# Optimization experiments

Measured on AMD Instinct MI355X. Metric: run time of the kernel, lower is better.

## Reference

```python
import jax, jax.numpy as jnp
import numpy as np

UNITS = 1024
HEADS = 16
DEPTH = UNITS // HEADS          # 64
REL_LEN = 64 + 1                # max_relative_position + 1
M = 2 * REL_LEN - 1             # 129 relative buckets (bidirectional)
B, L = 4, 1024


def setup_inputs() -> dict:
    key = jax.random.key(0)
    ks = jax.random.split(key, 8)
    s = 0.02
    x = jax.random.normal(ks[0], (B, L, UNITS), jnp.float32)
    wq = jax.random.normal(ks[1], (UNITS, UNITS), jnp.float32) * s
    wk = jax.random.normal(ks[2], (UNITS, UNITS), jnp.float32) * s
    wv = jax.random.normal(ks[3], (UNITS, UNITS), jnp.float32) * s
    wo = jax.random.normal(ks[4], (UNITS, UNITS), jnp.float32) * s
    bo = jnp.zeros((UNITS,), jnp.float32)
    ek = jax.random.normal(ks[5], (HEADS, M, DEPTH), jnp.float32) * s
    ev = jax.random.normal(ks[6], (HEADS, M, DEPTH), jnp.float32) * s
    pad_mask = jnp.zeros((B, 1, 1, L), jnp.float32)  # 1.0 where padded
    return dict(x=x, pad_mask=pad_mask, wq=wq, wk=wk, wv=wv, wo=wo, bo=bo, ek=ek, ev=ev)


def _rel_idx(length):
    # relative offset j - i, clipped to [-(REL_LEN-1), REL_LEN-1], shifted to [0, M-1].
    # Equivalent to the pad/reshape/slice skew trick: padding_relative_embeddings tiles the
    # edge embeddings (== clipping) and relative_to_absolute_pos realizes idx = j - i + REL_LEN - 1.
    i = jnp.arange(length)
    off = i[None, :] - i[:, None]
    return jnp.clip(off, -(REL_LEN - 1), REL_LEN - 1) + (REL_LEN - 1)  # [L, L] int32


def _forward(x, pad_mask, wq, wk, wv, wo, bo, ek, ev):
    b, length, _ = x.shape

    def split_heads(h):  # [B, L, U] -> [B, H, L, D]
        return jnp.transpose(h.reshape(b, length, HEADS, DEPTH), (0, 2, 1, 3))

    q = split_heads(x @ wq)
    k = split_heads(x @ wk)
    v = split_heads(x @ wv)

    idx = _rel_idx(length)                                   # [L, L]
    qk = jnp.einsum('bhid,bhjd->bhij', q, k)                 # [B, H, L, L]
    # relative key logits: q . E_k over relative buckets, then relative->absolute gather
    qm = jnp.einsum('bhld,hmd->bhlm', q, ek)                 # [B, H, L, M]
    rel_k = jnp.take_along_axis(qm, idx[None, None, :, :], axis=-1)  # [B, H, L, L]
    logits = (qk + rel_k) / jnp.sqrt(jnp.asarray(DEPTH, jnp.float32))
    logits = logits + pad_mask * -1e9
    attn = jax.nn.softmax(logits, axis=-1)                   # [B, H, L, L]
    out = jnp.einsum('bhij,bhjd->bhid', attn, v)             # [B, H, L, D]

    # value relative position: out[b,h,i,d] += sum_j attn[b,h,i,j] * E_v[h, idx[i,j], d]
    # Implemented by scattering attn into relative buckets (avoids the [H,L,L,D] tensor
    # the original materializes), mathematically identical.
    def per_query(attn_i, idx_i):  # attn_i [B, H, L], idx_i [L]
        return jax.ops.segment_sum(jnp.moveaxis(attn_i, -1, 0), idx_i, num_segments=M)  # [M, B, H]

    wr = jax.vmap(per_query, in_axes=(2, 0))(attn, idx)      # [L, M, B, H]
    wr = jnp.transpose(wr, (2, 3, 0, 1))                     # [B, H, L, M]
    out = out + jnp.einsum('bhlm,hmd->bhld', wr, ev)

    out = jnp.transpose(out, (0, 2, 1, 3)).reshape(b, length, UNITS)  # combine heads
    return out @ wo + bo


def reference(x, pad_mask, wq, wk, wv, wo, bo, ek, ev):
    return _forward(x, pad_mask, wq, wk, wv, wo, bo, ek, ev)
```

## Files before the change

kernel.cpp:

```cpp
#include <hip/hip_runtime.h>

typedef unsigned short u16;
typedef short s16x8 __attribute__((ext_vector_type(8)));
typedef float f32x4 __attribute__((ext_vector_type(4)));

static __device__ __forceinline__ u16 f2b(float f) {
  union { float f; unsigned u; } v; v.f = f;
  unsigned r = v.u + 0x7fffu + ((v.u >> 16) & 1u);
  return (u16)(r >> 16);
}
static __device__ __forceinline__ float b2f(u16 u) {
  union { unsigned u; float f; } v; v.u = ((unsigned)u) << 16;
  return v.f;
}

#define MFMA16(a, b, c) __builtin_amdgcn_mfma_f32_16x16x32_bf16((a), (b), (c), 0, 0, 0)

static __device__ __forceinline__ void gload_lds16(const u16* g, u16* l) {
  __builtin_amdgcn_global_load_lds((const __attribute__((address_space(1))) void*)g,
                                   (__attribute__((address_space(3))) void*)l, 16, 0, 0);
}

__global__ void k_cast_x(const float* __restrict__ src, u16* __restrict__ dst, int n4) {
  int i = blockIdx.x * blockDim.x + threadIdx.x;
  if (i >= n4) return;
  float4 v = ((const float4*)src)[i];
  ushort4 o;
  o.x = f2b(v.x); o.y = f2b(v.y); o.z = f2b(v.z); o.w = f2b(v.w);
  ((ushort4*)dst)[i] = o;
}

__global__ void k_transpose_w(const float* wq, const float* wk, const float* wv, const float* wo,
                              u16* dq, u16* dk, u16* dv, u16* dwo) {
  const float* src; u16* dst;
  int z = blockIdx.z;
  if (z == 0)      { src = wq; dst = dq; }
  else if (z == 1) { src = wk; dst = dk; }
  else if (z == 2) { src = wv; dst = dv; }
  else             { src = wo; dst = dwo; }
  __shared__ float t[32][33];
  int x0 = blockIdx.x * 32, y0 = blockIdx.y * 32;
  int tx = threadIdx.x, ty = threadIdx.y;
#pragma unroll
  for (int k = 0; k < 4; k++) t[ty + 8 * k][tx] = src[(size_t)(y0 + ty + 8 * k) * 1024 + x0 + tx];
  __syncthreads();
#pragma unroll
  for (int k = 0; k < 4; k++) dst[(size_t)(x0 + ty + 8 * k) * 1024 + y0 + tx] = f2b(t[tx][ty + 8 * k]);
}

__global__ void k_prep_rel(const float* __restrict__ ek, const float* __restrict__ ev,
                           u16* __restrict__ ekb, u16* __restrict__ evt) {
  int i = blockIdx.x * blockDim.x + threadIdx.x;
  if (i < 16 * 144 * 64) {
    int h = i / (144 * 64); int rem = i % (144 * 64); int m = rem / 64; int d = rem % 64;
    ekb[i] = (m < 129) ? f2b(ek[((size_t)h * 129 + m) * 64 + d]) : (u16)0;
  }
  if (i < 16 * 64 * 160) {
    int h = i / (64 * 160); int rem = i % (64 * 160); int d = rem / 160; int mm = rem % 160;
    evt[i] = (mm < 129) ? f2b(ev[((size_t)h * 129 + mm) * 64 + d]) : (u16)0;
  }
}

static __device__ __forceinline__ void gemm_body(const u16* __restrict__ A, const u16* __restrict__ Bt,
                                                 void* __restrict__ Cout, const float* __restrict__ bias,
                                                 int mode, int bx, int by) {
  __shared__ u16 As[128 * 32];
  __shared__ u16 Bs[128 * 32];
  int tid = threadIdx.x;
  int w = tid >> 6, lane = tid & 63;
  int wrw = w >> 1, wcw = w & 1, lr = lane & 15, lk = lane >> 4;
  int m0 = by * 128, n0 = bx * 128;
  f32x4 acc[4][4] = {};
  int crow = lane >> 2;
  int ccol = (lane & 3) * 8;
  const u16* gA = &A [(size_t)(m0 + w * 32 + crow) * 1024 + ccol];
  const u16* gB = &Bt[(size_t)(n0 + w * 32 + crow) * 1024 + ccol];
  u16* lA = &As[w * 32 * 32];
  u16* lB = &Bs[w * 32 * 32];
  for (int k0 = 0; k0 < 1024; k0 += 32) {
    __syncthreads();
    gload_lds16(gA + k0,             lA);
    gload_lds16(gA + k0 + 16 * 1024, lA + 16 * 32);
    gload_lds16(gB + k0,             lB);
    gload_lds16(gB + k0 + 16 * 1024, lB + 16 * 32);
    __syncthreads();
    s16x8 af[4], bfr[4];
#pragma unroll
    for (int mt = 0; mt < 4; mt++) af[mt]  = *(const s16x8*)&As[(wrw * 64 + mt * 16 + lr) * 32 + lk * 8];
#pragma unroll
    for (int nt = 0; nt < 4; nt++) bfr[nt] = *(const s16x8*)&Bs[(wcw * 64 + nt * 16 + lr) * 32 + lk * 8];
    __builtin_amdgcn_s_setprio(1);
#pragma unroll
    for (int mt = 0; mt < 4; mt++)
#pragma unroll
      for (int nt = 0; nt < 4; nt++)
        acc[mt][nt] = MFMA16(af[mt], bfr[nt], acc[mt][nt]);
    __builtin_amdgcn_s_setprio(0);
  }
#pragma unroll
  for (int mt = 0; mt < 4; mt++)
#pragma unroll
    for (int nt = 0; nt < 4; nt++)
#pragma unroll
      for (int r = 0; r < 4; r++) {
        int row = m0 + wrw * 64 + mt * 16 + lk * 4 + r;
        int col = n0 + wcw * 64 + nt * 16 + lr;
        float v = acc[mt][nt][r];
        if (mode == 2) {
          ((float*)Cout)[(size_t)row * 1024 + col] = v + bias[col];
        } else {
          int bb = row >> 10, l = row & 1023;
          int hh = col >> 6, dd = col & 63;
          if (mode == 0)
            ((u16*)Cout)[((size_t)(bb * 16 + hh)) * 65536 + (size_t)l * 64 + dd] = f2b(v);
          else
            ((u16*)Cout)[((size_t)(bb * 16 + hh)) * 65536 + (size_t)dd * 1024 + l] = f2b(v);
        }
      }
}

__global__ __launch_bounds__(256) void k_gemm_qkv(const u16* __restrict__ A,
                                                  const u16* __restrict__ BtQ, const u16* __restrict__ BtK,
                                                  const u16* __restrict__ BtV,
                                                  u16* __restrict__ Qo, u16* __restrict__ Ko,
                                                  u16* __restrict__ Vo) {
  int z = blockIdx.z;
  const u16* Bt = (z == 0) ? BtQ : (z == 1) ? BtK : BtV;
  u16* Cout     = (z == 0) ? Qo  : (z == 1) ? Ko  : Vo;
  gemm_body(A, Bt, Cout, nullptr, (z == 2) ? 1 : 0, blockIdx.x, blockIdx.y);
}

__global__ __launch_bounds__(256) void k_gemm_out(const u16* __restrict__ A, const u16* __restrict__ Bt,
                                                  float* __restrict__ Cout, const float* __restrict__ bias) {
  gemm_body(A, Bt, Cout, bias, 2, blockIdx.x, blockIdx.y);
}

#define THR_DM 8.0f
__global__ __launch_bounds__(256) void k_attn(const u16* __restrict__ Qg, const u16* __restrict__ Kg,
                                              const u16* __restrict__ Vt, const u16* __restrict__ ekb,
                                              const u16* __restrict__ evt, const float* __restrict__ pmask,
                                              u16* __restrict__ Og) {
  __shared__ alignas(16) char smem[73472];
  float* qm_s      = (float*)smem;
  u16*   P_s       = (u16*)(smem + 34048);
  u16*   wrb       = (u16*)(smem + 51456);
  float* row_scale = (float*)(smem + 72960);
  float* row_sum   = (float*)(smem + 73216);

  int tid = threadIdx.x, w = tid >> 6, lane = tid & 63, lr = lane & 15, lk = lane >> 4;
  int bh = blockIdx.x >> 4, it = blockIdx.x & 15;
  int b = bh >> 4, h = bh & 15;
  int i0 = it * 64;
  int i_base = w * 16 + lk * 4;

  for (int t = tid; t < 5376; t += 256) ((unsigned*)wrb)[t] = 0u;

  s16x8 aq[2];
  {
    const u16* qp = &Qg[((size_t)bh * 1024 + i0 + w * 16 + lr) * 64 + lk * 8];
    aq[0] = *(const s16x8*)qp; aq[1] = *(const s16x8*)(qp + 32);
  }

#pragma unroll
  for (int nt = 0; nt < 9; nt++) {
    f32x4 c = {};
    const u16* ekp = &ekb[((size_t)h * 144 + nt * 16 + lr) * 64 + lk * 8];
    c = MFMA16(aq[0], *(const s16x8*)ekp, c);
    c = MFMA16(aq[1], *(const s16x8*)(ekp + 32), c);
    int mcol = nt * 16 + lr;
    if (mcol < 133) {
#pragma unroll
      for (int r = 0; r < 4; r++) qm_s[(i_base + r) * 133 + mcol] = c[r];
    }
  }
  __syncthreads();

  float mrow[4] = {-3e38f, -3e38f, -3e38f, -3e38f};
  f32x4 oacc[4] = {};
  float lsum = 0.f, rsum = 0.f;
  int iw = tid >> 2, sub = tid & 3, ig = i0 + iw;

  for (int jt = 0; jt < 8; jt++) {
    int j0 = jt * 128;
    float mk[8];
#pragma unroll
    for (int nt = 0; nt < 8; nt++) mk[nt] = pmask[b * 1024 + j0 + nt * 16 + lr] * -1e9f;
    float sv[8][4];
#pragma unroll
    for (int nt = 0; nt < 8; nt++) {
      f32x4 c = {};
      const u16* kp = &Kg[((size_t)bh * 1024 + j0 + nt * 16 + lr) * 64 + lk * 8];
      c = MFMA16(aq[0], *(const s16x8*)kp, c);
      c = MFMA16(aq[1], *(const s16x8*)(kp + 32), c);
      int j = j0 + nt * 16 + lr;
#pragma unroll
      for (int r = 0; r < 4; r++) {
        int dl = j - (i0 + i_base + r);
        dl = dl < -64 ? -64 : (dl > 64 ? 64 : dl);
        sv[nt][r] = (c[r] + qm_s[(i_base + r) * 133 + dl + 64]) * 0.125f + mk[nt];
      }
    }
#pragma unroll
    for (int r = 0; r < 4; r++) {
      float mx = sv[0][r];
#pragma unroll
      for (int nt = 1; nt < 8; nt++) mx = fmaxf(mx, sv[nt][r]);
#pragma unroll
      for (int o = 1; o < 16; o <<= 1) mx = fmaxf(mx, __shfl_xor(mx, o));
      float sc = 1.0f;
      if (mx > mrow[r] + THR_DM) {
        sc = __expf(mrow[r] - mx);
        mrow[r] = mx;
#pragma unroll
        for (int nt = 0; nt < 4; nt++) oacc[nt][r] *= sc;
      }
      if (lr == 0) row_scale[i_base + r] = sc;
#pragma unroll
      for (int nt = 0; nt < 8; nt++)
        P_s[(i_base + r) * 136 + nt * 16 + lr] = f2b(__expf(sv[nt][r] - mrow[r]));
    }
    __syncthreads();

    __builtin_amdgcn_s_setprio(1);
    {
      s16x8 ap[4];
#pragma unroll
      for (int kk = 0; kk < 4; kk++) ap[kk] = *(const s16x8*)&P_s[(w * 16 + lr) * 136 + kk * 32 + lk * 8];
#pragma unroll
      for (int nt = 0; nt < 4; nt++) {
        const u16* vp = &Vt[((size_t)bh * 64 + nt * 16 + lr) * 1024 + j0 + lk * 8];
#pragma unroll
        for (int kk = 0; kk < 4; kk++)
          oacc[nt] = MFMA16(ap[kk], *(const s16x8*)(vp + kk * 32), oacc[nt]);
      }
    }
    __builtin_amdgcn_s_setprio(0);

    {
      float sc2 = row_scale[iw];
      if (sc2 != 1.0f) {
        lsum *= sc2; rsum *= sc2;
        unsigned* wrow = (unsigned*)&wrb[iw * 168];
        for (int t = sub; t < 84; t += 4) {
          unsigned vv = wrow[t];
          float lo = b2f((u16)(vv & 0xffffu)) * sc2;
          float hi = b2f((u16)(vv >> 16)) * sc2;
          wrow[t] = (unsigned)f2b(lo) | ((unsigned)f2b(hi) << 16);
        }
      }
      if (j0 + 127 < ig - 63) {
        float s = 0.f;
#pragma unroll
        for (int t = 0; t < 8; t++) {
          ushort4 pv = *(const ushort4*)&P_s[iw * 136 + sub * 32 + t * 4];
          s += b2f(pv.x) + b2f(pv.y) + b2f(pv.z) + b2f(pv.w);
        }
        lsum += s;
      } else if (j0 > ig + 63) {
        float s = 0.f;
#pragma unroll
        for (int t = 0; t < 8; t++) {
          ushort4 pv = *(const ushort4*)&P_s[iw * 136 + sub * 32 + t * 4];
          s += b2f(pv.x) + b2f(pv.y) + b2f(pv.z) + b2f(pv.w);
        }
        rsum += s;
      } else {
        for (int kk = 0; kk < 32; kk++) {
          int jj = kk * 4 + sub;
          float p = b2f(P_s[iw * 136 + jj]);
          int dl = (j0 + jj) - ig;
          if (dl <= -64) lsum += p;
          else if (dl >= 64) rsum += p;
          else wrb[iw * 168 + dl + 64] = f2b(p);
        }
      }
    }
    __syncthreads();
  }

  lsum += __shfl_xor(lsum, 1); lsum += __shfl_xor(lsum, 2);
  rsum += __shfl_xor(rsum, 1); rsum += __shfl_xor(rsum, 2);
  if (sub == 0) { wrb[iw * 168] = f2b(lsum); wrb[iw * 168 + 128] = f2b(rsum); }
  __syncthreads();

  {
    float s = 0.f;
#pragma unroll
    for (int t = 0; t < 10; t++) {
      ushort4 pv = *(const ushort4*)&wrb[iw * 168 + t * 16 + sub * 4];
      s += b2f(pv.x) + b2f(pv.y) + b2f(pv.z) + b2f(pv.w);
    }
    s += __shfl_xor(s, 1); s += __shfl_xor(s, 2);
    if (sub == 0) row_sum[iw] = s;
  }
  __syncthreads();

  __builtin_amdgcn_s_setprio(1);
  {
    s16x8 aw[5];
#pragma unroll
    for (int kk = 0; kk < 5; kk++) aw[kk] = *(const s16x8*)&wrb[(w * 16 + lr) * 168 + kk * 32 + lk * 8];
#pragma unroll
    for (int nt = 0; nt < 4; nt++) {
      const u16* ep = &evt[((size_t)h * 64 + nt * 16 + lr) * 160 + lk * 8];
#pragma unroll
      for (int kk = 0; kk < 5; kk++)
        oacc[nt] = MFMA16(aw[kk], *(const s16x8*)(ep + kk * 32), oacc[nt]);
    }
  }
  __builtin_amdgcn_s_setprio(0);

#pragma unroll
  for (int nt = 0; nt < 4; nt++)
#pragma unroll
    for (int r = 0; r < 4; r++) {
      int i_loc = i_base + r;
      float v = oacc[nt][r] / row_sum[i_loc];
      Og[((size_t)(b * 1024 + i0 + i_loc)) * 1024 + h * 64 + nt * 16 + lr] = f2b(v);
    }
}

#define OFF_XB   0u
#define OFF_WQT  8388608u
#define OFF_WKT  10485760u
#define OFF_WVT  12582912u
#define OFF_WOT  14680064u
#define OFF_Q    16777216u
#define OFF_K    25165824u
#define OFF_VT   33554432u
#define OFF_O    41943040u
#define OFF_EKB  50331648u
#define OFF_EVT  50626560u

extern "C" void kernel_launch(void* const* d_in, const int* in_sizes, int n_in,
                              void* d_out, int out_size, void* d_ws, size_t ws_size,
                              hipStream_t stream) {
  const float* x  = (const float*)d_in[0];
  const float* pm = (const float*)d_in[1];
  const float* wq = (const float*)d_in[2];
  const float* wk = (const float*)d_in[3];
  const float* wv = (const float*)d_in[4];
  const float* wo = (const float*)d_in[5];
  const float* bo = (const float*)d_in[6];
  const float* ek = (const float*)d_in[7];
  const float* ev = (const float*)d_in[8];
  char* ws = (char*)d_ws;
  u16* Xb  = (u16*)(ws + OFF_XB);
  u16* Wqt = (u16*)(ws + OFF_WQT);
  u16* Wkt = (u16*)(ws + OFF_WKT);
  u16* Wvt = (u16*)(ws + OFF_WVT);
  u16* Wot = (u16*)(ws + OFF_WOT);
  u16* Qg  = (u16*)(ws + OFF_Q);
  u16* Kg  = (u16*)(ws + OFF_K);
  u16* Vtg = (u16*)(ws + OFF_VT);
  u16* Og  = (u16*)(ws + OFF_O);
  u16* EKB = (u16*)(ws + OFF_EKB);
  u16* EVT = (u16*)(ws + OFF_EVT);

  k_cast_x<<<4096, 256, 0, stream>>>(x, Xb, 1048576);
  {
    dim3 tb(32, 8), tg(32, 32, 4);
    k_transpose_w<<<tg, tb, 0, stream>>>(wq, wk, wv, wo, Wqt, Wkt, Wvt, Wot);
  }
  k_prep_rel<<<640, 256, 0, stream>>>(ek, ev, EKB, EVT);
  {
    dim3 gq(8, 32, 3);
    k_gemm_qkv<<<gq, 256, 0, stream>>>(Xb, Wqt, Wkt, Wvt, Qg, Kg, Vtg);
    k_attn<<<1024, 256, 0, stream>>>(Qg, Kg, Vtg, EKB, EVT, pm, Og);
    dim3 go(8, 32);
    k_gemm_out<<<go, 256, 0, stream>>>(Og, Wot, (float*)d_out, bo);
  }
}
```

Before: 314.9 us.

## Rewrite attention as single-wave blocks without online max, split V GEMM

The attention kernel now runs as 4096 single-wavefront blocks of 16 query rows instead of 1024 four-wave blocks, so the per-tile __syncthreads barriers go away. The online-max rescaling is replaced by a direct exp with a clamp at 80, and the row sum is accumulated in registers. The relative-key logits and the mask are staged in LDS as bf16, and blocks are remapped across groups. The V projection moves to its own templated GEMM that swaps the MFMA operands so transposed stores are coalesced. Dropping max subtraction risks overflow or precision loss when logits are large, and bf16 qm adds rounding error.

```diff
diff --git a/kernel.cpp b/kernel.cpp
--- a/kernel.cpp
+++ b/kernel.cpp
@@ -61,9 +61,10 @@
   }
 }
 
+template <int MODE>
 static __device__ __forceinline__ void gemm_body(const u16* __restrict__ A, const u16* __restrict__ Bt,
                                                  void* __restrict__ Cout, const float* __restrict__ bias,
-                                                 int mode, int bx, int by) {
+                                                 int bx, int by) {
   __shared__ u16 As[128 * 32];
   __shared__ u16 Bs[128 * 32];
   int tid = threadIdx.x;
@@ -93,8 +94,10 @@
 #pragma unroll
     for (int mt = 0; mt < 4; mt++)
 #pragma unroll
-      for (int nt = 0; nt < 4; nt++)
-        acc[mt][nt] = MFMA16(af[mt], bfr[nt], acc[mt][nt]);
+      for (int nt = 0; nt < 4; nt++) {
+        if (MODE == 1) acc[mt][nt] = MFMA16(bfr[nt], af[mt], acc[mt][nt]);
+        else           acc[mt][nt] = MFMA16(af[mt], bfr[nt], acc[mt][nt]);
+      }
     __builtin_amdgcn_s_setprio(0);
   }
 #pragma unroll
@@ -103,206 +106,184 @@
     for (int nt = 0; nt < 4; nt++)
 #pragma unroll
       for (int r = 0; r < 4; r++) {
-        int row = m0 + wrw * 64 + mt * 16 + lk * 4 + r;
-        int col = n0 + wcw * 64 + nt * 16 + lr;
         float v = acc[mt][nt][r];
-        if (mode == 2) {
-          ((float*)Cout)[(size_t)row * 1024 + col] = v + bias[col];
+        if (MODE == 1) {
+          int u = n0 + wcw * 64 + nt * 16 + lk * 4 + r;
+          int l = m0 + wrw * 64 + mt * 16 + lr;
+          int bb = l >> 10, ll = l & 1023;
+          int hh = u >> 6, dd = u & 63;
+          ((u16*)Cout)[((size_t)(bb * 16 + hh)) * 65536 + (size_t)dd * 1024 + ll] = f2b(v);
         } else {
-          int bb = row >> 10, l = row & 1023;
-          int hh = col >> 6, dd = col & 63;
-          if (mode == 0)
+          int row = m0 + wrw * 64 + mt * 16 + lk * 4 + r;
+          int col = n0 + wcw * 64 + nt * 16 + lr;
+          if (MODE == 2) {
+            ((float*)Cout)[(size_t)row * 1024 + col] = v + bias[col];
+          } else {
+            int bb = row >> 10, l = row & 1023;
+            int hh = col >> 6, dd = col & 63;
             ((u16*)Cout)[((size_t)(bb * 16 + hh)) * 65536 + (size_t)l * 64 + dd] = f2b(v);
-          else
-            ((u16*)Cout)[((size_t)(bb * 16 + hh)) * 65536 + (size_t)dd * 1024 + l] = f2b(v);
+          }
         }
       }
 }
 
-__global__ __launch_bounds__(256) void k_gemm_qkv(const u16* __restrict__ A,
-                                                  const u16* __restrict__ BtQ, const u16* __restrict__ BtK,
-                                                  const u16* __restrict__ BtV,
-                                                  u16* __restrict__ Qo, u16* __restrict__ Ko,
-                                                  u16* __restrict__ Vo) {
-  int z = blockIdx.z;
-  const u16* Bt = (z == 0) ? BtQ : (z == 1) ? BtK : BtV;
-  u16* Cout     = (z == 0) ? Qo  : (z == 1) ? Ko  : Vo;
-  gemm_body(A, Bt, Cout, nullptr, (z == 2) ? 1 : 0, blockIdx.x, blockIdx.y);
-}
-
+__global__ __launch_bounds__(256) void k_gemm_qk(const u16* __restrict__ A,
+                                                 const u16* __restrict__ BtQ, const u16* __restrict__ BtK,
+                                                 u16* __restrict__ Qo, u16* __restrict__ Ko) {
+  const u16* Bt = blockIdx.z ? BtK : BtQ;
+  u16* C        = blockIdx.z ? Ko  : Qo;
+  gemm_body<0>(A, Bt, C, nullptr, blockIdx.x, blockIdx.y);
+}
+__global__ __launch_bounds__(256) void k_gemm_v(const u16* __restrict__ A, const u16* __restrict__ Bt,
+                                                u16* __restrict__ Vo) {
+  gemm_body<1>(A, Bt, Vo, nullptr, blockIdx.x, blockIdx.y);
+}
 __global__ __launch_bounds__(256) void k_gemm_out(const u16* __restrict__ A, const u16* __restrict__ Bt,
                                                   float* __restrict__ Cout, const float* __restrict__ bias) {
-  gemm_body(A, Bt, Cout, bias, 2, blockIdx.x, blockIdx.y);
-}
-
-#define THR_DM 8.0f
-__global__ __launch_bounds__(256) void k_attn(const u16* __restrict__ Qg, const u16* __restrict__ Kg,
-                                              const u16* __restrict__ Vt, const u16* __restrict__ ekb,
-                                              const u16* __restrict__ evt, const float* __restrict__ pmask,
-                                              u16* __restrict__ Og) {
-  __shared__ alignas(16) char smem[73472];
-  float* qm_s      = (float*)smem;
-  u16*   P_s       = (u16*)(smem + 34048);
-  u16*   wrb       = (u16*)(smem + 51456);
-  float* row_scale = (float*)(smem + 72960);
-  float* row_sum   = (float*)(smem + 73216);
-
-  int tid = threadIdx.x, w = tid >> 6, lane = tid & 63, lr = lane & 15, lk = lane >> 4;
-  int bh = blockIdx.x >> 4, it = blockIdx.x & 15;
+  gemm_body<2>(A, Bt, Cout, bias, blockIdx.x, blockIdx.y);
+}
+
+__global__ __launch_bounds__(64) void k_attn(const u16* __restrict__ Qg, const u16* __restrict__ Kg,
+                                             const u16* __restrict__ Vt, const u16* __restrict__ ekb,
+                                             const u16* __restrict__ evt, const float* __restrict__ pmask,
+                                             u16* __restrict__ Og) {
+  __shared__ alignas(16) char smem[16128];
+  u16* qm_s   = (u16*)smem;
+  u16* P_s    = (u16*)(smem + 4352);
+  u16* wrb    = (u16*)(smem + 8704);
+  u16* mask_s = (u16*)(smem + 14080);
+
+  int lane = threadIdx.x;
+  int lr = lane & 15, lk = lane >> 4;
+  int wg = (blockIdx.x & 7) * 512 + (blockIdx.x >> 3);
+  int bh = wg >> 6, it = wg & 63;
   int b = bh >> 4, h = bh & 15;
-  int i0 = it * 64;
-  int i_base = w * 16 + lk * 4;
-
-  for (int t = tid; t < 5376; t += 256) ((unsigned*)wrb)[t] = 0u;
-
-  s16x8 aq[2];
+  int i0 = it * 16;
+
   {
-    const u16* qp = &Qg[((size_t)bh * 1024 + i0 + w * 16 + lr) * 64 + lk * 8];
-    aq[0] = *(const s16x8*)qp; aq[1] = *(const s16x8*)(qp + 32);
-  }
+    const float4* pm4 = (const float4*)(pmask + (size_t)b * 1024);
+#pragma unroll
+    for (int t = 0; t < 4; t++) {
+      float4 v = pm4[lane * 4 + t];
+      unsigned w0 = (unsigned)f2b(v.x * -1e9f) | ((unsigned)f2b(v.y * -1e9f) << 16);
+      unsigned w1 = (unsigned)f2b(v.z * -1e9f) | ((unsigned)f2b(v.w * -1e9f) << 16);
+      ((unsigned*)mask_s)[lane * 8 + t * 2]     = w0;
+      ((unsigned*)mask_s)[lane * 8 + t * 2 + 1] = w1;
+    }
+  }
+  for (int t = lane; t < 1344; t += 64) ((unsigned*)wrb)[t] = 0u;
+
+  const u16* qp = &Qg[((size_t)bh * 1024 + i0 + lr) * 64 + lk * 8];
+  s16x8 aq0 = *(const s16x8*)qp;
+  s16x8 aq1 = *(const s16x8*)(qp + 32);
 
 #pragma unroll
   for (int nt = 0; nt < 9; nt++) {
     f32x4 c = {};
     const u16* ekp = &ekb[((size_t)h * 144 + nt * 16 + lr) * 64 + lk * 8];
-    c = MFMA16(aq[0], *(const s16x8*)ekp, c);
-    c = MFMA16(aq[1], *(const s16x8*)(ekp + 32), c);
+    c = MFMA16(aq0, *(const s16x8*)ekp, c);
+    c = MFMA16(aq1, *(const s16x8*)(ekp + 32), c);
     int mcol = nt * 16 + lr;
-    if (mcol < 133) {
-#pragma unroll
-      for (int r = 0; r < 4; r++) qm_s[(i_base + r) * 133 + mcol] = c[r];
-    }
-  }
-  __syncthreads();
-
-  float mrow[4] = {-3e38f, -3e38f, -3e38f, -3e38f};
+    if (mcol < 129) {
+#pragma unroll
+      for (int r = 0; r < 4; r++) qm_s[(lk * 4 + r) * 136 + mcol] = f2b(c[r]);
+    }
+  }
+
+  float ssum = 0.f, lsum = 0.f, rsum = 0.f;
   f32x4 oacc[4] = {};
-  float lsum = 0.f, rsum = 0.f;
-  int iw = tid >> 2, sub = tid & 3, ig = i0 + iw;
+  const int ig = i0 + lr;
 
   for (int jt = 0; jt < 8; jt++) {
     int j0 = jt * 128;
-    float mk[8];
-#pragma unroll
-    for (int nt = 0; nt < 8; nt++) mk[nt] = pmask[b * 1024 + j0 + nt * 16 + lr] * -1e9f;
-    float sv[8][4];
+    float p[8][4];
+    const u16* kbase = &Kg[((size_t)bh * 1024 + j0 + lr) * 64 + lk * 8];
 #pragma unroll
     for (int nt = 0; nt < 8; nt++) {
       f32x4 c = {};
-      const u16* kp = &Kg[((size_t)bh * 1024 + j0 + nt * 16 + lr) * 64 + lk * 8];
-      c = MFMA16(aq[0], *(const s16x8*)kp, c);
-      c = MFMA16(aq[1], *(const s16x8*)(kp + 32), c);
-      int j = j0 + nt * 16 + lr;
+      const u16* kp = kbase + nt * 16 * 64;
+      c = MFMA16(*(const s16x8*)kp, aq0, c);
+      c = MFMA16(*(const s16x8*)(kp + 32), aq1, c);
 #pragma unroll
       for (int r = 0; r < 4; r++) {
-        int dl = j - (i0 + i_base + r);
+        int j = j0 + nt * 16 + lk * 4 + r;
+        int dl = j - ig;
         dl = dl < -64 ? -64 : (dl > 64 ? 64 : dl);
-        sv[nt][r] = (c[r] + qm_s[(i_base + r) * 133 + dl + 64]) * 0.125f + mk[nt];
-      }
-    }
-#pragma unroll
-    for (int r = 0; r < 4; r++) {
-      float mx = sv[0][r];
-#pragma unroll
-      for (int nt = 1; nt < 8; nt++) mx = fmaxf(mx, sv[nt][r]);
-#pragma unroll
-      for (int o = 1; o < 16; o <<= 1) mx = fmaxf(mx, __shfl_xor(mx, o));
-      float sc = 1.0f;
-      if (mx > mrow[r] + THR_DM) {
-        sc = __expf(mrow[r] - mx);
-        mrow[r] = mx;
-#pragma unroll
-        for (int nt = 0; nt < 4; nt++) oacc[nt][r] *= sc;
-      }
-      if (lr == 0) row_scale[i_base + r] = sc;
-#pragma unroll
-      for (int nt = 0; nt < 8; nt++)
-        P_s[(i_base + r) * 136 + nt * 16 + lr] = f2b(__expf(sv[nt][r] - mrow[r]));
-    }
-    __syncthreads();
-
+        float qmv = b2f(qm_s[lr * 136 + dl + 64]);
+        float madd = b2f(mask_s[j]);
+        float sval = fminf((c[r] + qmv) * 0.125f + madd, 80.f);
+        float pv = __expf(sval);
+        p[nt][r] = pv;
+        ssum += pv;
+      }
+    }
+#pragma unroll
+    for (int nt = 0; nt < 8; nt++) {
+      unsigned lo, hi;
+      asm("v_cvt_pk_bf16_f32 %0, %1, %2" : "=v"(lo) : "v"(p[nt][0]), "v"(p[nt][1]));
+      asm("v_cvt_pk_bf16_f32 %0, %1, %2" : "=v"(hi) : "v"(p[nt][2]), "v"(p[nt][3]));
+      uint2 pk; pk.x = lo; pk.y = hi;
+      *(uint2*)&P_s[lr * 136 + nt * 16 + lk * 4] = pk;
+    }
     __builtin_amdgcn_s_setprio(1);
     {
       s16x8 ap[4];
 #pragma unroll
-      for (int kk = 0; kk < 4; kk++) ap[kk] = *(const s16x8*)&P_s[(w * 16 + lr) * 136 + kk * 32 + lk * 8];
+      for (int kk = 0; kk < 4; kk++) ap[kk] = *(const s16x8*)&P_s[lr * 136 + kk * 32 + lk * 8];
+      const u16* vbase = &Vt[((size_t)bh * 64 + lr) * 1024 + j0 + lk * 8];
 #pragma unroll
       for (int nt = 0; nt < 4; nt++) {
-        const u16* vp = &Vt[((size_t)bh * 64 + nt * 16 + lr) * 1024 + j0 + lk * 8];
+        const u16* vp = vbase + nt * 16 * 1024;
 #pragma unroll
         for (int kk = 0; kk < 4; kk++)
           oacc[nt] = MFMA16(ap[kk], *(const s16x8*)(vp + kk * 32), oacc[nt]);
       }
     }
     __builtin_amdgcn_s_setprio(0);
-
     {
-      float sc2 = row_scale[iw];
-      if (sc2 != 1.0f) {
-        lsum *= sc2; rsum *= sc2;
-        unsigned* wrow = (unsigned*)&wrb[iw * 168];
-        for (int t = sub; t < 84; t += 4) {
-          unsigned vv = wrow[t];
-          float lo = b2f((u16)(vv & 0xffffu)) * sc2;
-          float hi = b2f((u16)(vv >> 16)) * sc2;
-          wrow[t] = (unsigned)f2b(lo) | ((unsigned)f2b(hi) << 16);
-        }
-      }
-      if (j0 + 127 < ig - 63) {
+      int jmin = j0 + lk * 4;
+      int jmax = j0 + 112 + lk * 4 + 3;
+      if (jmax <= ig - 64) {
         float s = 0.f;
 #pragma unroll
-        for (int t = 0; t < 8; t++) {
-          ushort4 pv = *(const ushort4*)&P_s[iw * 136 + sub * 32 + t * 4];
-          s += b2f(pv.x) + b2f(pv.y) + b2f(pv.z) + b2f(pv.w);
-        }
+        for (int nt = 0; nt < 8; nt++) s += (p[nt][0] + p[nt][1]) + (p[nt][2] + p[nt][3]);
         lsum += s;
-      } else if (j0 > ig + 63) {
+      } else if (jmin >= ig + 64) {
         float s = 0.f;
 #pragma unroll
-        for (int t = 0; t < 8; t++) {
-          ushort4 pv = *(const ushort4*)&P_s[iw * 136 + sub * 32 + t * 4];
-          s += b2f(pv.x) + b2f(pv.y) + b2f(pv.z) + b2f(pv.w);
-        }
+        for (int nt = 0; nt < 8; nt++) s += (p[nt][0] + p[nt][1]) + (p[nt][2] + p[nt][3]);
         rsum += s;
       } else {
-        for (int kk = 0; kk < 32; kk++) {
-          int jj = kk * 4 + sub;
-          float p = b2f(P_s[iw * 136 + jj]);
-          int dl = (j0 + jj) - ig;
-          if (dl <= -64) lsum += p;
-          else if (dl >= 64) rsum += p;
-          else wrb[iw * 168 + dl + 64] = f2b(p);
-        }
-      }
-    }
-    __syncthreads();
-  }
-
-  lsum += __shfl_xor(lsum, 1); lsum += __shfl_xor(lsum, 2);
-  rsum += __shfl_xor(rsum, 1); rsum += __shfl_xor(rsum, 2);
-  if (sub == 0) { wrb[iw * 168] = f2b(lsum); wrb[iw * 168 + 128] = f2b(rsum); }
-  __syncthreads();
-
-  {
-    float s = 0.f;
-#pragma unroll
-    for (int t = 0; t < 10; t++) {
-      ushort4 pv = *(const ushort4*)&wrb[iw * 168 + t * 16 + sub * 4];
-      s += b2f(pv.x) + b2f(pv.y) + b2f(pv.z) + b2f(pv.w);
-    }
-    s += __shfl_xor(s, 1); s += __shfl_xor(s, 2);
-    if (sub == 0) row_sum[iw] = s;
-  }
-  __syncthreads();
+#pragma unroll
+        for (int nt = 0; nt < 8; nt++)
+#pragma unroll
+          for (int r = 0; r < 4; r++) {
+            int dl = j0 + nt * 16 + lk * 4 + r - ig;
+            if (dl <= -64) lsum += p[nt][r];
+            else if (dl >= 64) rsum += p[nt][r];
+            else wrb[lr * 168 + dl + 64] = f2b(p[nt][r]);
+          }
+      }
+    }
+  }
+
+  lsum += __shfl_xor(lsum, 16); lsum += __shfl_xor(lsum, 32);
+  rsum += __shfl_xor(rsum, 16); rsum += __shfl_xor(rsum, 32);
+  ssum += __shfl_xor(ssum, 16); ssum += __shfl_xor(ssum, 32);
+  if (lk == 0) {
+    wrb[lr * 168]       = f2b(lsum);
+    wrb[lr * 168 + 128] = f2b(rsum);
+  }
 
   __builtin_amdgcn_s_setprio(1);
   {
     s16x8 aw[5];
 #pragma unroll
-    for (int kk = 0; kk < 5; kk++) aw[kk] = *(const s16x8*)&wrb[(w * 16 + lr) * 168 + kk * 32 + lk * 8];
+    for (int kk = 0; kk < 5; kk++) aw[kk] = *(const s16x8*)&wrb[lr * 168 + kk * 32 + lk * 8];
+    const u16* ebase = &evt[((size_t)h * 64 + lr) * 160 + lk * 8];
 #pragma unroll
     for (int nt = 0; nt < 4; nt++) {
-      const u16* ep = &evt[((size_t)h * 64 + nt * 16 + lr) * 160 + lk * 8];
+      const u16* ep = ebase + nt * 16 * 160;
 #pragma unroll
       for (int kk = 0; kk < 5; kk++)
         oacc[nt] = MFMA16(aw[kk], *(const s16x8*)(ep + kk * 32), oacc[nt]);
@@ -310,13 +291,16 @@
   }
   __builtin_amdgcn_s_setprio(0);
 
+  float rden[4];
+#pragma unroll
+  for (int r = 0; r < 4; r++) rden[r] = 1.0f / __shfl(ssum, lk * 4 + r);
+  u16* obase = &Og[((size_t)(b * 1024 + i0)) * 1024 + h * 64];
 #pragma unroll
   for (int nt = 0; nt < 4; nt++)
 #pragma unroll
     for (int r = 0; r < 4; r++) {
-      int i_loc = i_base + r;
-      float v = oacc[nt][r] / row_sum[i_loc];
-      Og[((size_t)(b * 1024 + i0 + i_loc)) * 1024 + h * 64 + nt * 16 + lr] = f2b(v);
+      int il = lk * 4 + r;
+      obase[(size_t)il * 1024 + nt * 16 + lr] = f2b(oacc[nt][r] * rden[r]);
     }
 }
 
@@ -364,9 +348,11 @@
   }
   k_prep_rel<<<640, 256, 0, stream>>>(ek, ev, EKB, EVT);
   {
-    dim3 gq(8, 32, 3);
-    k_gemm_qkv<<<gq, 256, 0, stream>>>(Xb, Wqt, Wkt, Wvt, Qg, Kg, Vtg);
-    k_attn<<<1024, 256, 0, stream>>>(Qg, Kg, Vtg, EKB, EVT, pm, Og);
+    dim3 gqk(8, 32, 2);
+    k_gemm_qk<<<gqk, 256, 0, stream>>>(Xb, Wqt, Wkt, Qg, Kg);
+    dim3 gv(8, 32);
+    k_gemm_v<<<gv, 256, 0, stream>>>(Xb, Wvt, Vtg);
+    k_attn<<<4096, 64, 0, stream>>>(Qg, Kg, Vtg, EKB, EVT, pm, Og);
     dim3 go(8, 32);
     k_gemm_out<<<go, 256, 0, stream>>>(Og, Wot, (float*)d_out, bo);
   }
```

Measured after the change: 319.7 us. About the same (+1.5%).
